# Optimization experiments

Hardware: AMD Instinct MI355X
Metric: run time of the kernel (lower is better)

## Reference

```python
import jax, jax.numpy as jnp
import numpy as np


def _directional_scan(x_steps, alpha_b, reverse):
    """x_steps: (S, B, C, L); alpha_b: (1, C, 1). Returns (S, B, C, L).
    Recurrence: cur = relu(x_s + alpha * prev), prev0 = 0  (equivalent to the
    original's first-step special case since alpha*0 == 0)."""
    def step(prev, xs):
        cur = jax.nn.relu(xs + alpha_b * prev)
        return cur, cur
    init = jnp.zeros_like(x_steps[0])
    _, ys = jax.lax.scan(step, init, x_steps, reverse=reverse)
    return ys


def setup_inputs() -> dict:
    key = jax.random.key(0)
    k1, k2 = jax.random.split(key)
    B, C, H, W = 8, 32, 256, 256
    x = jax.random.normal(k1, (B, C, H, W), dtype=jnp.float32)
    alpha = jnp.full((C,), 0.2, dtype=jnp.float32)
    return {"x": x, "alpha": alpha}


def reference(x, alpha):
    # x: (B, C, H, W); alpha: (C,)
    alpha_b = alpha.reshape(1, -1, 1)  # broadcast over (B, C, L)
    x_h = jnp.moveaxis(x, 2, 0)  # (H, B, C, W)
    h_td = jnp.moveaxis(_directional_scan(x_h, alpha_b, reverse=False), 0, 2)
    h_dt = jnp.moveaxis(_directional_scan(x_h, alpha_b, reverse=True), 0, 2)
    x_w = jnp.moveaxis(x, 3, 0)  # (W, B, C, H)
    h_lr = jnp.moveaxis(_directional_scan(x_w, alpha_b, reverse=False), 0, 3)
    h_rl = jnp.moveaxis(_directional_scan(x_w, alpha_b, reverse=True), 0, 3)
    return (h_td, h_lr, h_dt, h_rl)
```

## Files before the change

### kernel.cpp

```cpp
#include <hip/hip_runtime.h>

#define BB 8
#define CC 32
#define HH 256
#define WW 256
#define SEG 64
#define HALO 16
#define NPLANE (BB*CC)
#define PLANE_ELEMS (HH*WW)

__global__ __launch_bounds__(256) void vert_kernel(
    const float* __restrict__ x, const float* __restrict__ alpha,
    float* __restrict__ out_td, float* __restrict__ out_dt) {
  int blk = blockIdx.x;
  int seg = blk & 3;
  int plane = blk >> 2;
  int c = plane & (CC - 1);
  float a = alpha[c];
  int w = threadIdx.x;
  const float* xp = x + (size_t)plane * PLANE_ELEMS + w;
  float* otd = out_td + (size_t)plane * PLANE_ELEMS + w;
  float* odt = out_dt + (size_t)plane * PLANE_ELEMS + w;
  int h0 = seg * SEG;

  {
    int hs = h0 - HALO; if (hs < 0) hs = 0;
    float prev = 0.f;
    for (int h = hs; h < h0; ++h) {
      prev = fmaxf(fmaf(a, prev, xp[h * WW]), 0.f);
    }
#pragma unroll 8
    for (int h = h0; h < h0 + SEG; ++h) {
      prev = fmaxf(fmaf(a, prev, xp[h * WW]), 0.f);
      otd[h * WW] = prev;
    }
  }
  {
    int hs = h0 + SEG - 1 + HALO; if (hs > HH - 1) hs = HH - 1;
    float prev = 0.f;
    for (int h = hs; h >= h0 + SEG; --h) {
      prev = fmaxf(fmaf(a, prev, xp[h * WW]), 0.f);
    }
#pragma unroll 8
    for (int h = h0 + SEG - 1; h >= h0; --h) {
      prev = fmaxf(fmaf(a, prev, xp[h * WW]), 0.f);
      odt[h * WW] = prev;
    }
  }
}

#define TSTRIDE 257
__global__ __launch_bounds__(256) void horiz_kernel(
    const float* __restrict__ x, const float* __restrict__ alpha,
    float* __restrict__ out_lr, float* __restrict__ out_rl) {
  __shared__ float tile[64 * TSTRIDE];
  int blk = blockIdx.x;
  int rg = blk & 3;
  int plane = blk >> 2;
  int c = plane & (CC - 1);
  float a = alpha[c];
  const float* xp = x + (size_t)plane * PLANE_ELEMS + rg * 64 * WW;
  float* olr = out_lr + (size_t)plane * PLANE_ELEMS + rg * 64 * WW;
  float* orl = out_rl + (size_t)plane * PLANE_ELEMS + rg * 64 * WW;
  int t = threadIdx.x;
  int r = t & 63;
  int s = t >> 6;
  int c0 = s * SEG;

#pragma unroll 16
  for (int i = 0; i < 64; ++i) {
    tile[i * TSTRIDE + t] = xp[i * WW + t];
  }
  __syncthreads();

  {
    float prev = 0.f;
    int cs = c0 - HALO; if (cs < 0) cs = 0;
    for (int cc = cs; cc < c0; ++cc)
      prev = fmaxf(fmaf(a, prev, tile[r * TSTRIDE + cc]), 0.f);
    __syncthreads();
#pragma unroll 8
    for (int cc = c0; cc < c0 + SEG; ++cc) {
      prev = fmaxf(fmaf(a, prev, tile[r * TSTRIDE + cc]), 0.f);
      tile[r * TSTRIDE + cc] = prev;
    }
  }
  __syncthreads();

#pragma unroll 16
  for (int i = 0; i < 64; ++i) {
    int idx = i * TSTRIDE + t;
    olr[i * WW + t] = tile[idx];
    tile[idx] = xp[i * WW + t];
  }
  __syncthreads();

  {
    float prev = 0.f;
    int cs = c0 + SEG - 1 + HALO; if (cs > WW - 1) cs = WW - 1;
    for (int cc = cs; cc > c0 + SEG - 1; --cc)
      prev = fmaxf(fmaf(a, prev, tile[r * TSTRIDE + cc]), 0.f);
    __syncthreads();
#pragma unroll 8
    for (int cc = c0 + SEG - 1; cc >= c0; --cc) {
      prev = fmaxf(fmaf(a, prev, tile[r * TSTRIDE + cc]), 0.f);
      tile[r * TSTRIDE + cc] = prev;
    }
  }
  __syncthreads();

#pragma unroll 16
  for (int i = 0; i < 64; ++i) {
    orl[i * WW + t] = tile[i * TSTRIDE + t];
  }
}

extern "C" void kernel_launch(void* const* d_in, const int* in_sizes, int n_in,
                              void* d_out, int out_size, void* d_ws, size_t ws_size,
                              hipStream_t stream) {
  const float* x = (const float*)d_in[0];
  const float* alpha = (const float*)d_in[1];
  float* out = (float*)d_out;
  const size_t N = (size_t)BB * CC * HH * WW;
  float* out_td = out;
  float* out_lr = out + N;
  float* out_dt = out + 2 * N;
  float* out_rl = out + 3 * N;

  vert_kernel<<<NPLANE * (HH / SEG), 256, 0, stream>>>(x, alpha, out_td, out_dt);
  horiz_kernel<<<NPLANE * (HH / 64), 256, 0, stream>>>(x, alpha, out_lr, out_rl);
}
```

Baseline: 337.3 us.

## Fuse vertical and horizontal scans into one kernel sharing the LDS tile

Merges the vertical and horizontal scan kernels into a single kernel. Each block loads its 64-row band into LDS once and runs the top-down and bottom-up scans from LDS, reading only the 16-row halos from global memory. The global loads and stores for the horizontal pass now use float4, and the horizontal halo warm-up is hoisted so both directions' halos are read before the tile is overwritten. This removes the vertical kernel's separate reads of x, at the cost of roughly 64KB of LDS per block limiting occupancy and a longer serial path inside each block.

```diff
diff --git a/kernel.cpp b/kernel.cpp
--- a/kernel.cpp
+++ b/kernel.cpp
@@ -4,114 +4,115 @@
 #define CC 32
 #define HH 256
 #define WW 256
-#define SEG 64
+#define NPLANE (BB*CC)
+#define PLANE 65536
+#define TSTRIDE 257
 #define HALO 16
-#define NPLANE (BB*CC)
-#define PLANE_ELEMS (HH*WW)
 
-__global__ __launch_bounds__(256) void vert_kernel(
+__global__ __launch_bounds__(256, 2) void fused_kernel(
     const float* __restrict__ x, const float* __restrict__ alpha,
-    float* __restrict__ out_td, float* __restrict__ out_dt) {
-  int blk = blockIdx.x;
-  int seg = blk & 3;
-  int plane = blk >> 2;
-  int c = plane & (CC - 1);
-  float a = alpha[c];
-  int w = threadIdx.x;
-  const float* xp = x + (size_t)plane * PLANE_ELEMS + w;
-  float* otd = out_td + (size_t)plane * PLANE_ELEMS + w;
-  float* odt = out_dt + (size_t)plane * PLANE_ELEMS + w;
-  int h0 = seg * SEG;
+    float* __restrict__ otd, float* __restrict__ olr,
+    float* __restrict__ odt, float* __restrict__ orl) {
+  __shared__ float tile[64 * TSTRIDE];
+  const int blk = blockIdx.x;
+  const int rg = blk & 3;
+  const int plane = blk >> 2;
+  const float a = alpha[plane & (CC - 1)];
+  const int t = threadIdx.x;
 
-  {
-    int hs = h0 - HALO; if (hs < 0) hs = 0;
-    float prev = 0.f;
-    for (int h = hs; h < h0; ++h) {
-      prev = fmaxf(fmaf(a, prev, xp[h * WW]), 0.f);
-    }
-#pragma unroll 8
-    for (int h = h0; h < h0 + SEG; ++h) {
-      prev = fmaxf(fmaf(a, prev, xp[h * WW]), 0.f);
-      otd[h * WW] = prev;
-    }
-  }
-  {
-    int hs = h0 + SEG - 1 + HALO; if (hs > HH - 1) hs = HH - 1;
-    float prev = 0.f;
-    for (int h = hs; h >= h0 + SEG; --h) {
-      prev = fmaxf(fmaf(a, prev, xp[h * WW]), 0.f);
-    }
-#pragma unroll 8
-    for (int h = h0 + SEG - 1; h >= h0; --h) {
-      prev = fmaxf(fmaf(a, prev, xp[h * WW]), 0.f);
-      odt[h * WW] = prev;
-    }
-  }
-}
+  const size_t pbase = (size_t)plane * PLANE + (size_t)rg * 64 * WW;
+  const float* xp = x + pbase;
+  float* ptd = otd + pbase;
+  float* plr = olr + pbase;
+  float* pdt = odt + pbase;
+  float* prl = orl + pbase;
 
-#define TSTRIDE 257
-__global__ __launch_bounds__(256) void horiz_kernel(
-    const float* __restrict__ x, const float* __restrict__ alpha,
-    float* __restrict__ out_lr, float* __restrict__ out_rl) {
-  __shared__ float tile[64 * TSTRIDE];
-  int blk = blockIdx.x;
-  int rg = blk & 3;
-  int plane = blk >> 2;
-  int c = plane & (CC - 1);
-  float a = alpha[c];
-  const float* xp = x + (size_t)plane * PLANE_ELEMS + rg * 64 * WW;
-  float* olr = out_lr + (size_t)plane * PLANE_ELEMS + rg * 64 * WW;
-  float* orl = out_rl + (size_t)plane * PLANE_ELEMS + rg * 64 * WW;
-  int t = threadIdx.x;
-  int r = t & 63;
-  int s = t >> 6;
-  int c0 = s * SEG;
+  const int r4 = t >> 6;
+  const int c4 = t & 63;
 
-#pragma unroll 16
-  for (int i = 0; i < 64; ++i) {
-    tile[i * TSTRIDE + t] = xp[i * WW + t];
+#pragma unroll
+  for (int i = 0; i < 16; ++i) {
+    int row = i * 4 + r4;
+    float4 v = ((const float4*)(xp + row * WW))[c4];
+    float* dst = &tile[row * TSTRIDE + 4 * c4];
+    dst[0] = v.x; dst[1] = v.y; dst[2] = v.z; dst[3] = v.w;
   }
   __syncthreads();
 
   {
     float prev = 0.f;
-    int cs = c0 - HALO; if (cs < 0) cs = 0;
-    for (int cc = cs; cc < c0; ++cc)
-      prev = fmaxf(fmaf(a, prev, tile[r * TSTRIDE + cc]), 0.f);
-    __syncthreads();
+    if (rg > 0) {
+      const float* hp = x + (size_t)plane * PLANE + (size_t)(rg * 64 - HALO) * WW + t;
+#pragma unroll
+      for (int i = 0; i < HALO; ++i)
+        prev = fmaxf(fmaf(a, prev, hp[i * WW]), 0.f);
+    }
 #pragma unroll 8
-    for (int cc = c0; cc < c0 + SEG; ++cc) {
-      prev = fmaxf(fmaf(a, prev, tile[r * TSTRIDE + cc]), 0.f);
-      tile[r * TSTRIDE + cc] = prev;
+    for (int i = 0; i < 64; ++i) {
+      prev = fmaxf(fmaf(a, prev, tile[i * TSTRIDE + t]), 0.f);
+      ptd[i * WW + t] = prev;
     }
+    prev = 0.f;
+    if (rg < 3) {
+      const float* hp = x + (size_t)plane * PLANE + (size_t)(rg * 64 + 64) * WW + t;
+#pragma unroll
+      for (int i = HALO - 1; i >= 0; --i)
+        prev = fmaxf(fmaf(a, prev, hp[i * WW]), 0.f);
+    }
+#pragma unroll 8
+    for (int i = 63; i >= 0; --i) {
+      prev = fmaxf(fmaf(a, prev, tile[i * TSTRIDE + t]), 0.f);
+      pdt[i * WW + t] = prev;
+    }
+  }
+
+  const int r = t & 63;
+  const int s = t >> 6;
+  const int c0 = s * 64;
+  float prev_lr = 0.f, prev_rl = 0.f;
+  if (s > 0) {
+#pragma unroll
+    for (int cc = c0 - HALO; cc < c0; ++cc)
+      prev_lr = fmaxf(fmaf(a, prev_lr, tile[r * TSTRIDE + cc]), 0.f);
+  }
+  if (s < 3) {
+#pragma unroll
+    for (int cc = c0 + 64 + HALO - 1; cc >= c0 + 64; --cc)
+      prev_rl = fmaxf(fmaf(a, prev_rl, tile[r * TSTRIDE + cc]), 0.f);
   }
   __syncthreads();
 
-#pragma unroll 16
-  for (int i = 0; i < 64; ++i) {
-    int idx = i * TSTRIDE + t;
-    olr[i * WW + t] = tile[idx];
-    tile[idx] = xp[i * WW + t];
+#pragma unroll 8
+  for (int cc = c0; cc < c0 + 64; ++cc) {
+    prev_lr = fmaxf(fmaf(a, prev_lr, tile[r * TSTRIDE + cc]), 0.f);
+    tile[r * TSTRIDE + cc] = prev_lr;
   }
   __syncthreads();
 
-  {
-    float prev = 0.f;
-    int cs = c0 + SEG - 1 + HALO; if (cs > WW - 1) cs = WW - 1;
-    for (int cc = cs; cc > c0 + SEG - 1; --cc)
-      prev = fmaxf(fmaf(a, prev, tile[r * TSTRIDE + cc]), 0.f);
-    __syncthreads();
-#pragma unroll 8
-    for (int cc = c0 + SEG - 1; cc >= c0; --cc) {
-      prev = fmaxf(fmaf(a, prev, tile[r * TSTRIDE + cc]), 0.f);
-      tile[r * TSTRIDE + cc] = prev;
-    }
+#pragma unroll
+  for (int i = 0; i < 16; ++i) {
+    int row = i * 4 + r4;
+    float* cell = &tile[row * TSTRIDE + 4 * c4];
+    float4 v; v.x = cell[0]; v.y = cell[1]; v.z = cell[2]; v.w = cell[3];
+    ((float4*)(plr + row * WW))[c4] = v;
+    float4 xv = ((const float4*)(xp + row * WW))[c4];
+    cell[0] = xv.x; cell[1] = xv.y; cell[2] = xv.z; cell[3] = xv.w;
   }
   __syncthreads();
 
-#pragma unroll 16
-  for (int i = 0; i < 64; ++i) {
-    orl[i * WW + t] = tile[i * TSTRIDE + t];
+#pragma unroll 8
+  for (int cc = c0 + 63; cc >= c0; --cc) {
+    prev_rl = fmaxf(fmaf(a, prev_rl, tile[r * TSTRIDE + cc]), 0.f);
+    tile[r * TSTRIDE + cc] = prev_rl;
+  }
+  __syncthreads();
+
+#pragma unroll
+  for (int i = 0; i < 16; ++i) {
+    int row = i * 4 + r4;
+    float* cell = &tile[row * TSTRIDE + 4 * c4];
+    float4 v; v.x = cell[0]; v.y = cell[1]; v.z = cell[2]; v.w = cell[3];
+    ((float4*)(prl + row * WW))[c4] = v;
   }
 }
 
@@ -127,6 +128,6 @@
   float* out_dt = out + 2 * N;
   float* out_rl = out + 3 * N;
 
-  vert_kernel<<<NPLANE * (HH / SEG), 256, 0, stream>>>(x, alpha, out_td, out_dt);
-  horiz_kernel<<<NPLANE * (HH / 64), 256, 0, stream>>>(x, alpha, out_lr, out_rl);
+  fused_kernel<<<NPLANE * (HH / 64), 256, 0, stream>>>(
+      x, alpha, out_td, out_lr, out_dt, out_rl);
 }
```

Result: faster. 313.8 us (-7.0%).
